# Optimization experiments

Measured on AMD Instinct MI355X. Metric: run time of the kernel, lower is better.

The kernel has to match this reference:

```python
import jax, jax.numpy as jnp
import numpy as np

B, L, F, H = 8, 1024, 1024, 16
D = F // H  # head dim = 64

def setup_inputs() -> dict:
    key = jax.random.key(0)
    k1, k2, k3, k4 = jax.random.split(key, 4)
    x = jax.random.normal(k1, (B, L, F), jnp.float32)
    # lecun_normal-style scaling for projections
    w_qkv = jax.random.normal(k2, (F, 3 * F), jnp.float32) / jnp.sqrt(F)
    # relative position bias table: (2*window-1, heads)
    rpe_table = jax.random.normal(k3, (2 * L - 1, H), jnp.float32) * 0.02
    w_out = jax.random.normal(k4, (F, F), jnp.float32) / jnp.sqrt(F)
    return {"x": x, "w_qkv": w_qkv, "rpe_table": rpe_table, "w_out": w_out}

def reference(x, w_qkv, rpe_table, w_out):
    # QKV projection (use_bias=False)
    qkv = jnp.einsum('blf,fe->ble', x, w_qkv)              # [B, L, 3F]
    qkv = qkv.reshape(B, L, H, 3 * D)
    q, k, v = jnp.split(qkv, 3, axis=-1)                   # each [B, L, H, D]
    q = q / jnp.sqrt(jnp.asarray(D, x.dtype))
    # relative positional bias: gather table at index (i - j + L - 1)
    rel_idx = jnp.arange(L)[:, None] - jnp.arange(L)[None, :] + (L - 1)  # [L, L]
    bias = jnp.transpose(rpe_table[rel_idx], (2, 0, 1))    # [H, L, L]
    scores = jnp.einsum('bqhd,bkhd->bhqk', q, k) + bias[None]  # [B, H, L, L]
    attn = jax.nn.softmax(scores, axis=-1)
    out = jnp.einsum('bhqk,bkhd->bqhd', attn, v)           # [B, L, H, D]
    out = out.reshape(B, L, F)
    return jnp.einsum('blf,fo->blo', out, w_out)
```

## Files before the change

### kernel.cpp

```cpp
#include <hip/hip_runtime.h>


typedef __attribute__((ext_vector_type(8))) short bf16x8;
typedef __attribute__((ext_vector_type(4))) float f32x4;
typedef unsigned short u16;
typedef unsigned int u32;

__device__ __forceinline__ u16 f2bf(float f) {
  u32 u = __builtin_bit_cast(u32, f);
  u = (u + 0x7fffu + ((u >> 16) & 1u)) >> 16;
  return (u16)u;
}

__device__ __forceinline__ f32x4 mfma16(bf16x8 a, bf16x8 b, f32x4 c) {
  return __builtin_amdgcn_mfma_f32_16x16x32_bf16(a, b, c, 0, 0, 0);
}

__device__ __forceinline__ void gld_lds16(const u16* g, u16* l) {
  __builtin_amdgcn_global_load_lds(
      (const __attribute__((address_space(1))) unsigned int*)g,
      (__attribute__((address_space(3))) unsigned int*)l, 16, 0, 0);
}

__global__ __launch_bounds__(256) void cast_kernel(const float* __restrict__ in,
                                                   u16* __restrict__ out, int n8) {
  int i = blockIdx.x * 256 + threadIdx.x;
  if (i >= n8) return;
  float4 a = ((const float4*)in)[2 * i];
  float4 b = ((const float4*)in)[2 * i + 1];
  uint4 o;
  o.x = (u32)f2bf(a.x) | ((u32)f2bf(a.y) << 16);
  o.y = (u32)f2bf(a.z) | ((u32)f2bf(a.w) << 16);
  o.z = (u32)f2bf(b.x) | ((u32)f2bf(b.y) << 16);
  o.w = (u32)f2bf(b.z) | ((u32)f2bf(b.w) << 16);
  ((uint4*)out)[i] = o;
}

__global__ __launch_bounds__(256) void transpose_cast_kernel(const float* __restrict__ in,
                                                             u16* __restrict__ out,
                                                             int R, int C) {
  __shared__ float tile[32][33];
  const int c0 = blockIdx.x * 32, r0 = blockIdx.y * 32;
  const int tx = threadIdx.x, ty = threadIdx.y;
#pragma unroll
  for (int i = 0; i < 32; i += 8)
    tile[ty + i][tx] = in[(size_t)(r0 + ty + i) * C + (c0 + tx)];
  __syncthreads();
#pragma unroll
  for (int i = 0; i < 32; i += 8)
    out[(size_t)(c0 + ty + i) * R + (r0 + tx)] = f2bf(tile[tx][ty + i]);
}

__global__ __launch_bounds__(256) void rpe_prep_kernel(const float* __restrict__ rpe,
                                                       float* __restrict__ rpeT) {
  int o = blockIdx.x * 256 + threadIdx.x;
  int h = o >> 11, i = o & 2047;
  if (i < 2047) rpeT[h * 2048 + i] = rpe[(size_t)i * 16 + h] * 1.44269504f;
}

template <int EPI>
__global__ __launch_bounds__(256) void gemm_kernel(const u16* __restrict__ A,
                                                   const u16* __restrict__ BT,
                                                   void* __restrict__ C0,
                                                   void* __restrict__ C1,
                                                   int M, int N, int K) {
  __shared__ u16 As[128][64];
  __shared__ u16 Bs[128][64];
  const int tid = threadIdx.x;
  const int lane = tid & 63, w = tid >> 6;
  const int wrow = w >> 1, wcol = w & 1;
  const int bm0 = blockIdx.y * 128, bn0 = blockIdx.x * 128;
  const int l15 = lane & 15, l4 = lane >> 4;
  const int lr = lane >> 3, lc = (lane & 7) * 8;

  const f32x4 zero = {0.f, 0.f, 0.f, 0.f};
  f32x4 acc[4][4];
  for (int i = 0; i < 4; ++i)
    for (int j = 0; j < 4; ++j) acc[i][j] = zero;

  for (int k0 = 0; k0 < K; k0 += 64) {
    __syncthreads();
#pragma unroll
    for (int j = 0; j < 4; ++j) {
      int chunk = w * 4 + j;
      int r = chunk * 8 + lr;
      gld_lds16(A + (size_t)(bm0 + r) * K + k0 + lc, &As[0][0] + chunk * 512);
      gld_lds16(BT + (size_t)(bn0 + r) * K + k0 + lc, &Bs[0][0] + chunk * 512);
    }
    __syncthreads();
#pragma unroll
    for (int ks = 0; ks < 2; ++ks) {
      bf16x8 afr[4], bfr[4];
#pragma unroll
      for (int mi = 0; mi < 4; ++mi)
        afr[mi] = *(const bf16x8*)&As[wrow * 64 + mi * 16 + l15][ks * 32 + l4 * 8];
#pragma unroll
      for (int ni = 0; ni < 4; ++ni)
        bfr[ni] = *(const bf16x8*)&Bs[wcol * 64 + ni * 16 + l15][ks * 32 + l4 * 8];
#pragma unroll
      for (int mi = 0; mi < 4; ++mi)
#pragma unroll
        for (int ni = 0; ni < 4; ++ni)
          acc[mi][ni] = mfma16(afr[mi], bfr[ni], acc[mi][ni]);
    }
  }

  const int rbase = bm0 + wrow * 64 + l4 * 4;
  const int cbase = bn0 + wcol * 64 + l15;
  if constexpr (EPI == 1) {
    float* C = (float*)C0;
#pragma unroll
    for (int mi = 0; mi < 4; ++mi)
#pragma unroll
      for (int reg = 0; reg < 4; ++reg)
#pragma unroll
        for (int ni = 0; ni < 4; ++ni)
          C[(size_t)(rbase + mi * 16 + reg) * N + cbase + ni * 16] = acc[mi][ni][reg];
  } else {
    __syncthreads();
    u16* qkb = (u16*)C0;
    u16* vT = (u16*)C1;
    const int bq = bm0 >> 10;
    u16* buf = &As[0][0] + w * 1024;
#pragma unroll
    for (int ni = 0; ni < 4; ++ni) {
      int n16 = bn0 + wcol * 64 + ni * 16;
      int h = n16 / 192, sub = n16 - h * 192;
      if (sub < 128) {
#pragma unroll
        for (int mi = 0; mi < 4; ++mi)
#pragma unroll
          for (int reg = 0; reg < 4; ++reg) {
            int row = rbase + mi * 16 + reg;
            qkb[(size_t)row * 2048 + h * 128 + sub + l15] = f2bf(acc[mi][ni][reg]);
          }
      } else {
        asm volatile("s_waitcnt lgkmcnt(0)" ::: "memory");
#pragma unroll
        for (int mi = 0; mi < 4; ++mi)
#pragma unroll
          for (int reg = 0; reg < 4; ++reg) {
            int ml = mi * 16 + l4 * 4 + reg;
            buf[l15 * 64 + (((ml >> 3) ^ (l15 & 7)) * 8) + (ml & 7)] =
                f2bf(acc[mi][ni][reg]);
          }
        asm volatile("s_waitcnt lgkmcnt(0)" ::: "memory");
        int dbase = sub - 128;
#pragma unroll
        for (int pass = 0; pass < 2; ++pass) {
          int nl = lane >> 2, c2 = (lane & 3) + pass * 4;
          uint4 val = *(uint4*)&buf[nl * 64 + ((c2 ^ (nl & 7)) * 8)];
          int m = bm0 + wrow * 64 + c2 * 8;
          *(uint4*)&vT[(((size_t)(bq * 16 + h) * 64 + (dbase + nl)) << 10) + (m & 1023)] =
              val;
        }
      }
    }
  }
}

__global__ __launch_bounds__(512, 4) void attn_kernel(const u16* __restrict__ qk,
                                                      const u16* __restrict__ vT,
                                                      const float* __restrict__ rpeT,
                                                      u16* __restrict__ attn_out) {
  __shared__ u16 Ks[128][64];
  __shared__ u16 Vs[64][128];
  __shared__ u16 Ps[8][16][128];
  __shared__ float rpe_s[1152];

  const int tid = threadIdx.x, lane = tid & 63, w = tid >> 6;
  const int l15 = lane & 15, l4 = lane >> 4;
  const int bid = blockIdx.x;
  const int qt = bid >> 7, bh = bid & 127;
  const int h = bh & 15, b = bh >> 4;
  const int q0 = qt * 128;

  for (int t = tid; t < 1151; t += 512)
    rpe_s[t] = rpeT[h * 2048 + q0 + t];

  const u16* qbase = qk + ((size_t)(b * 1024 + q0 + w * 16 + l15) * 2048 + h * 128);
  bf16x8 bq0 = *(const bf16x8*)(qbase + l4 * 8);
  bf16x8 bq1 = *(const bf16x8*)(qbase + 32 + l4 * 8);

  const f32x4 zero = {0.f, 0.f, 0.f, 0.f};
  float m_run = -1e30f, l_run = 0.f;
  f32x4 oacc[4];
#pragma unroll
  for (int i = 0; i < 4; ++i) oacc[i] = zero;

  const u16* kgbase = qk + ((size_t)(b * 1024) * 2048 + h * 128 + 64);
  const u16* vgbase = vT + (size_t)bh * 65536;

  for (int kt = 0; kt < 8; ++kt) {
    const int kv0 = kt * 128;
    __syncthreads();
#pragma unroll
    for (int p = 0; p < 2; ++p) {
      int e = p * 512 + tid;
      int kr = e >> 3, kc = e & 7;
      gld_lds16(kgbase + (size_t)(kv0 + kr) * 2048 + ((kc ^ (kr & 7)) * 8),
                &Ks[0][0] + (size_t)(p * 512 + w * 64) * 8);
      int vr = e >> 4, vc = e & 15;
      gld_lds16(vgbase + (size_t)vr * 1024 + kv0 + ((vc ^ (vr & 7)) * 8),
                &Vs[0][0] + (size_t)(p * 512 + w * 64) * 8);
    }
    __syncthreads();

    f32x4 s[8];
    __builtin_amdgcn_s_setprio(1);
#pragma unroll
    for (int jt = 0; jt < 8; ++jt) {
      f32x4 t = zero;
      bf16x8 ak0 = *(const bf16x8*)&Ks[jt * 16 + l15][((l4) ^ (l15 & 7)) * 8];
      bf16x8 ak1 = *(const bf16x8*)&Ks[jt * 16 + l15][((4 + l4) ^ (l15 & 7)) * 8];
      t = mfma16(ak0, bq0, t);
      t = mfma16(ak1, bq1, t);
      s[jt] = t;
    }
    __builtin_amdgcn_s_setprio(0);

    const int ibase = w * 16 + l15 + 1023 - kv0 - l4 * 4;
#pragma unroll
    for (int jt = 0; jt < 8; ++jt)
#pragma unroll
      for (int reg = 0; reg < 4; ++reg)
        s[jt][reg] = s[jt][reg] * (0.125f * 1.44269504f) + rpe_s[ibase - jt * 16 - reg];

    float rm = fmaxf(fmaxf(s[0][0], s[0][1]), fmaxf(s[0][2], s[0][3]));
#pragma unroll
    for (int jt = 1; jt < 8; ++jt)
      rm = fmaxf(rm, fmaxf(fmaxf(s[jt][0], s[jt][1]), fmaxf(s[jt][2], s[jt][3])));
    rm = fmaxf(rm, __shfl_xor(rm, 16));
    rm = fmaxf(rm, __shfl_xor(rm, 32));

    if (__any(rm > m_run)) {
      float mnew = fmaxf(m_run, rm);
      float sc = __builtin_amdgcn_exp2f(m_run - mnew);
      m_run = mnew;
      l_run *= sc;
#pragma unroll
      for (int reg = 0; reg < 4; ++reg) {
        float scr = __shfl(sc, l4 * 4 + reg);
#pragma unroll
        for (int dt = 0; dt < 4; ++dt) oacc[dt][reg] *= scr;
      }
    }

    float rsum = 0.f;
#pragma unroll
    for (int jt = 0; jt < 8; ++jt) {
      float p0 = __builtin_amdgcn_exp2f(s[jt][0] - m_run);
      float p1 = __builtin_amdgcn_exp2f(s[jt][1] - m_run);
      float p2 = __builtin_amdgcn_exp2f(s[jt][2] - m_run);
      float p3 = __builtin_amdgcn_exp2f(s[jt][3] - m_run);
      rsum += (p0 + p1) + (p2 + p3);
      u32 pk01, pk23;
      asm("v_cvt_pk_bf16_f32 %0, %1, %2" : "=v"(pk01) : "v"(p0), "v"(p1));
      asm("v_cvt_pk_bf16_f32 %0, %1, %2" : "=v"(pk23) : "v"(p2), "v"(p3));
      int chunk = (jt * 2 + (l4 >> 1)) ^ (l15 & 7);
      u32* dst = (u32*)&Ps[w][l15][chunk * 8 + (l4 & 1) * 4];
      dst[0] = pk01;
      dst[1] = pk23;
    }
    rsum += __shfl_xor(rsum, 16);
    rsum += __shfl_xor(rsum, 32);
    l_run += rsum;

    __builtin_amdgcn_s_setprio(1);
#pragma unroll
    for (int ksv = 0; ksv < 4; ++ksv) {
      bf16x8 pa = *(const bf16x8*)&Ps[w][l15][((ksv * 4 + l4) ^ (l15 & 7)) * 8];
#pragma unroll
      for (int dt = 0; dt < 4; ++dt) {
        bf16x8 vb = *(const bf16x8*)&Vs[dt * 16 + l15][((ksv * 4 + l4) ^ (l15 & 7)) * 8];
        oacc[dt] = mfma16(pa, vb, oacc[dt]);
      }
    }
    __builtin_amdgcn_s_setprio(0);
  }

  float inv = 1.f / l_run;
#pragma unroll
  for (int reg = 0; reg < 4; ++reg) {
    float invr = __shfl(inv, l4 * 4 + reg);
    int row = b * 1024 + q0 + w * 16 + l4 * 4 + reg;
#pragma unroll
    for (int dt = 0; dt < 4; ++dt)
      attn_out[(size_t)row * 1024 + h * 64 + dt * 16 + l15] = f2bf(oacc[dt][reg] * invr);
  }
}

extern "C" void kernel_launch(void* const* d_in, const int* in_sizes, int n_in,
                              void* d_out, int out_size, void* d_ws, size_t ws_size,
                              hipStream_t stream) {
  const float* x     = (const float*)d_in[0];
  const float* w_qkv = (const float*)d_in[1];
  const float* rpe   = (const float*)d_in[2];
  const float* w_out = (const float*)d_in[3];

  char* ws = (char*)d_ws;
  u16* xb    = (u16*)(ws);
  u16* attnb = (u16*)(ws);
  u16* wqkvT = (u16*)(ws + 16777216);
  u16* woutT = (u16*)(ws + 23068672);
  float* rpeT = (float*)(ws + 23068672);
  u16* qkbuf = (u16*)(ws + 25165824);
  u16* vTbuf = (u16*)(ws + 58720256);

  cast_kernel<<<4096, 256, 0, stream>>>(x, xb, 8192 * 1024 / 8);
  dim3 tb(32, 8);
  transpose_cast_kernel<<<dim3(3072 / 32, 1024 / 32), tb, 0, stream>>>(w_qkv, wqkvT, 1024, 3072);
  rpe_prep_kernel<<<128, 256, 0, stream>>>(rpe, rpeT);

  gemm_kernel<0><<<dim3(3072 / 128, 8192 / 128), 256, 0, stream>>>(
      xb, wqkvT, (void*)qkbuf, (void*)vTbuf, 8192, 3072, 1024);

  attn_kernel<<<1024, 512, 0, stream>>>(qkbuf, vTbuf, rpeT, attnb);

  transpose_cast_kernel<<<dim3(1024 / 32, 1024 / 32), tb, 0, stream>>>(w_out, woutT, 1024, 1024);

  gemm_kernel<1><<<dim3(1024 / 128, 8192 / 128), 256, 0, stream>>>(
      attnb, woutT, d_out, nullptr, 8192, 1024, 1024);
}
```

Measured before the change: 267.8 us.

## Replace GEMM with 256x256 double-buffered pipelined kernel using swizzled LDS

The 128x128 single-buffered GEMM is replaced with a 512-thread kernel that computes 256x256 tiles. It double-buffers LDS, issues async global-to-LDS loads interleaved with MFMA quadrants under finer barriers and vmcnt waits, and XOR-swizzles LDS to avoid bank conflicts. It also remaps block IDs for XCD locality and raises MFMA wave priority. The aim is to overlap memory with compute and raise data reuse per tile. In exchange it uses more registers and LDS, and the larger tiles leave fewer workgroups (384 and 128) to fill the GPU.

Measured after the change: 265.9 us. No clear change (-0.7%).

```diff
diff --git a/kernel.cpp b/kernel.cpp
--- a/kernel.cpp
+++ b/kernel.cpp
@@ -21,6 +21,10 @@
       (const __attribute__((address_space(1))) unsigned int*)g,
       (__attribute__((address_space(3))) unsigned int*)l, 16, 0, 0);
 }
+
+#define BARRIER() asm volatile("s_barrier" ::: "memory")
+#define VMCNT4() asm volatile("s_waitcnt vmcnt(4)" ::: "memory")
+#define VMCNT0() asm volatile("s_waitcnt vmcnt(0)" ::: "memory")
 
 __global__ __launch_bounds__(256) void cast_kernel(const float* __restrict__ in,
                                                    u16* __restrict__ out, int n8) {
@@ -59,76 +63,144 @@
 }
 
 template <int EPI>
-__global__ __launch_bounds__(256) void gemm_kernel(const u16* __restrict__ A,
-                                                   const u16* __restrict__ BT,
-                                                   void* __restrict__ C0,
-                                                   void* __restrict__ C1,
-                                                   int M, int N, int K) {
-  __shared__ u16 As[128][64];
-  __shared__ u16 Bs[128][64];
-  const int tid = threadIdx.x;
-  const int lane = tid & 63, w = tid >> 6;
-  const int wrow = w >> 1, wcol = w & 1;
-  const int bm0 = blockIdx.y * 128, bn0 = blockIdx.x * 128;
+__global__ __launch_bounds__(512, 2) void gemm2_kernel(const u16* __restrict__ A,
+                                                       const u16* __restrict__ BT,
+                                                       void* __restrict__ C0,
+                                                       void* __restrict__ C1,
+                                                       int M, int N, int K, int ny) {
+  __shared__ u16 LA[2][256][64];
+  __shared__ u16 LB[2][256][64];
+  const int tid = threadIdx.x, lane = tid & 63, w = tid >> 6;
+  const int wm = w >> 2, wn = w & 3;
   const int l15 = lane & 15, l4 = lane >> 4;
-  const int lr = lane >> 3, lc = (lane & 7) * 8;
+  const int e7 = l15 & 7;
+
+  const int nwg = gridDim.x;
+  const int virt = ((int)blockIdx.x & 7) * (nwg >> 3) + ((int)blockIdx.x >> 3);
+  const int bx = virt / ny, by = virt % ny;
+  const int bm0 = by * 256, bn0 = bx * 256;
+  const int nt = K >> 6;
+
+  const int sr = tid >> 3, sc = tid & 7;
+
+  auto stageA = [&](int buf, int half, int kt) {
+#pragma unroll
+    for (int s = 0; s < 2; ++s) {
+      int r = s * 64 + sr;
+      gld_lds16(A + (size_t)(bm0 + half * 128 + r) * K + kt * 64 + ((sc ^ (r & 7)) * 8),
+                &LA[buf][half * 128][0] + s * 4096 + tid * 8);
+    }
+  };
+  auto stageB = [&](int buf, int half, int kt) {
+#pragma unroll
+    for (int s = 0; s < 2; ++s) {
+      int r = s * 64 + sr;
+      gld_lds16(BT + (size_t)(bn0 + half * 128 + r) * K + kt * 64 + ((sc ^ (r & 7)) * 8),
+                &LB[buf][half * 128][0] + s * 4096 + tid * 8);
+    }
+  };
 
   const f32x4 zero = {0.f, 0.f, 0.f, 0.f};
-  f32x4 acc[4][4];
-  for (int i = 0; i < 4; ++i)
+  f32x4 acc[8][4];
+#pragma unroll
+  for (int i = 0; i < 8; ++i)
+#pragma unroll
     for (int j = 0; j < 4; ++j) acc[i][j] = zero;
 
-  for (int k0 = 0; k0 < K; k0 += 64) {
-    __syncthreads();
-#pragma unroll
-    for (int j = 0; j < 4; ++j) {
-      int chunk = w * 4 + j;
-      int r = chunk * 8 + lr;
-      gld_lds16(A + (size_t)(bm0 + r) * K + k0 + lc, &As[0][0] + chunk * 512);
-      gld_lds16(BT + (size_t)(bn0 + r) * K + k0 + lc, &Bs[0][0] + chunk * 512);
-    }
-    __syncthreads();
-#pragma unroll
-    for (int ks = 0; ks < 2; ++ks) {
-      bf16x8 afr[4], bfr[4];
-#pragma unroll
-      for (int mi = 0; mi < 4; ++mi)
-        afr[mi] = *(const bf16x8*)&As[wrow * 64 + mi * 16 + l15][ks * 32 + l4 * 8];
-#pragma unroll
-      for (int ni = 0; ni < 4; ++ni)
-        bfr[ni] = *(const bf16x8*)&Bs[wcol * 64 + ni * 16 + l15][ks * 32 + l4 * 8];
-#pragma unroll
-      for (int mi = 0; mi < 4; ++mi)
-#pragma unroll
-        for (int ni = 0; ni < 4; ++ni)
-          acc[mi][ni] = mfma16(afr[mi], bfr[ni], acc[mi][ni]);
-    }
-  }
-
-  const int rbase = bm0 + wrow * 64 + l4 * 4;
-  const int cbase = bn0 + wcol * 64 + l15;
+  bf16x8 afr[8], bf0[4], bf1[4];
+
+  auto ldA = [&](int bt, int mh) {
+#pragma unroll
+    for (int mi2 = 0; mi2 < 4; ++mi2)
+#pragma unroll
+      for (int ks = 0; ks < 2; ++ks)
+        afr[mi2 * 2 + ks] = *(const bf16x8*)&LA[bt][wm * 128 + mh * 64 + mi2 * 16 + l15]
+                                               [((ks * 4 + l4) ^ e7) * 8];
+  };
+  auto ldB = [&](int bt, int nh, bf16x8* bfr) {
+#pragma unroll
+    for (int ni2 = 0; ni2 < 2; ++ni2)
+#pragma unroll
+      for (int ks = 0; ks < 2; ++ks)
+        bfr[ni2 * 2 + ks] = *(const bf16x8*)&LB[bt][wn * 64 + (nh * 2 + ni2) * 16 + l15]
+                                                [((ks * 4 + l4) ^ e7) * 8];
+  };
+  auto quad = [&](int mh, int nh, bf16x8* bfr) {
+    __builtin_amdgcn_s_setprio(1);
+#pragma unroll
+    for (int mi2 = 0; mi2 < 4; ++mi2)
+#pragma unroll
+      for (int ni2 = 0; ni2 < 2; ++ni2)
+#pragma unroll
+        for (int ks = 0; ks < 2; ++ks)
+          acc[mh * 4 + mi2][nh * 2 + ni2] =
+              mfma16(afr[mi2 * 2 + ks], bfr[ni2 * 2 + ks], acc[mh * 4 + mi2][nh * 2 + ni2]);
+    __builtin_amdgcn_s_setprio(0);
+  };
+
+  stageA(0, 0, 0);
+  stageA(0, 1, 0);
+  stageB(0, 0, 0);
+  stageB(0, 1, 0);
+  if (nt > 1) {
+    stageB(1, 0, 1);
+    stageB(1, 1, 1);
+  }
+  VMCNT4();
+  BARRIER();
+
+  for (int t = 0; t < nt; ++t) {
+    const int bt = t & 1;
+    ldA(bt, 0);
+    ldB(bt, 0, bf0);
+    if (t + 1 < nt) stageA(bt ^ 1, 0, t + 1);
+    BARRIER();
+    quad(0, 0, bf0);
+    BARRIER();
+    ldB(bt, 1, bf1);
+    if (t + 1 < nt) stageA(bt ^ 1, 1, t + 1);
+    BARRIER();
+    quad(0, 1, bf1);
+    BARRIER();
+    ldA(bt, 1);
+    if (t + 2 < nt) stageB(bt, 0, t + 2);
+    BARRIER();
+    quad(1, 0, bf0);
+    BARRIER();
+    if (t + 2 < nt) stageB(bt, 1, t + 2);
+    if (t < nt - 2) {
+      VMCNT4();
+    } else {
+      VMCNT0();
+    }
+    BARRIER();
+    quad(1, 1, bf1);
+    BARRIER();
+  }
+
+  const int rbase = bm0 + wm * 128 + l4 * 4;
+  const int cbase = bn0 + wn * 64 + l15;
   if constexpr (EPI == 1) {
     float* C = (float*)C0;
 #pragma unroll
-    for (int mi = 0; mi < 4; ++mi)
+    for (int mi = 0; mi < 8; ++mi)
 #pragma unroll
       for (int reg = 0; reg < 4; ++reg)
 #pragma unroll
         for (int ni = 0; ni < 4; ++ni)
           C[(size_t)(rbase + mi * 16 + reg) * N + cbase + ni * 16] = acc[mi][ni][reg];
   } else {
-    __syncthreads();
     u16* qkb = (u16*)C0;
     u16* vT = (u16*)C1;
     const int bq = bm0 >> 10;
-    u16* buf = &As[0][0] + w * 1024;
+    u16* bbuf = &LA[0][0][0] + w * 2048;
 #pragma unroll
     for (int ni = 0; ni < 4; ++ni) {
-      int n16 = bn0 + wcol * 64 + ni * 16;
+      int n16 = bn0 + wn * 64 + ni * 16;
       int h = n16 / 192, sub = n16 - h * 192;
       if (sub < 128) {
 #pragma unroll
-        for (int mi = 0; mi < 4; ++mi)
+        for (int mi = 0; mi < 8; ++mi)
 #pragma unroll
           for (int reg = 0; reg < 4; ++reg) {
             int row = rbase + mi * 16 + reg;
@@ -137,21 +209,20 @@
       } else {
         asm volatile("s_waitcnt lgkmcnt(0)" ::: "memory");
 #pragma unroll
-        for (int mi = 0; mi < 4; ++mi)
+        for (int mi = 0; mi < 8; ++mi)
 #pragma unroll
           for (int reg = 0; reg < 4; ++reg) {
             int ml = mi * 16 + l4 * 4 + reg;
-            buf[l15 * 64 + (((ml >> 3) ^ (l15 & 7)) * 8) + (ml & 7)] =
-                f2bf(acc[mi][ni][reg]);
+            bbuf[l15 * 128 + (((ml >> 3) ^ e7) * 8) + (ml & 7)] = f2bf(acc[mi][ni][reg]);
           }
         asm volatile("s_waitcnt lgkmcnt(0)" ::: "memory");
-        int dbase = sub - 128;
-#pragma unroll
-        for (int pass = 0; pass < 2; ++pass) {
-          int nl = lane >> 2, c2 = (lane & 3) + pass * 4;
-          uint4 val = *(uint4*)&buf[nl * 64 + ((c2 ^ (nl & 7)) * 8)];
-          int m = bm0 + wrow * 64 + c2 * 8;
-          *(uint4*)&vT[(((size_t)(bq * 16 + h) * 64 + (dbase + nl)) << 10) + (m & 1023)] =
+        int dsub = sub - 128;
+#pragma unroll
+        for (int pass = 0; pass < 4; ++pass) {
+          int nl = lane >> 2, cc = (lane & 3) + pass * 4;
+          uint4 val = *(uint4*)&bbuf[nl * 128 + ((cc ^ (nl & 7)) * 8)];
+          int mg = bm0 + wm * 128 + cc * 8;
+          *(uint4*)&vT[(((size_t)(bq * 16 + h) * 64 + (dsub + nl)) << 10) + (mg & 1023)] =
               val;
         }
       }
@@ -312,13 +383,13 @@
   transpose_cast_kernel<<<dim3(3072 / 32, 1024 / 32), tb, 0, stream>>>(w_qkv, wqkvT, 1024, 3072);
   rpe_prep_kernel<<<128, 256, 0, stream>>>(rpe, rpeT);
 
-  gemm_kernel<0><<<dim3(3072 / 128, 8192 / 128), 256, 0, stream>>>(
-      xb, wqkvT, (void*)qkbuf, (void*)vTbuf, 8192, 3072, 1024);
+  gemm2_kernel<0><<<384, 512, 0, stream>>>(xb, wqkvT, (void*)qkbuf, (void*)vTbuf,
+                                           8192, 3072, 1024, 32);
 
   attn_kernel<<<1024, 512, 0, stream>>>(qkbuf, vTbuf, rpeT, attnb);
 
   transpose_cast_kernel<<<dim3(1024 / 32, 1024 / 32), tb, 0, stream>>>(w_out, woutT, 1024, 1024);
 
-  gemm_kernel<1><<<dim3(1024 / 128, 8192 / 128), 256, 0, stream>>>(
-      attnb, woutT, d_out, nullptr, 8192, 1024, 1024);
-}
+  gemm2_kernel<1><<<128, 512, 0, stream>>>(attnb, woutT, d_out, nullptr,
+                                           8192, 1024, 1024, 32);
+}
```
